# Kernel optimization log

Hardware: AMD Instinct MI355X
Metric: run time of the kernel (lower is better)

Reference implementation:

```python
import jax, jax.numpy as jnp
import numpy as np

L = 8        # num_layers
B = 4        # batch
S = 1024     # seq_len
D = 1024     # hidden_size
H = 16       # num_heads
FC = 4096    # fc_size
NEG = -1e9   # additive causal-mask value (matches torch code's -1000000000.0)


def setup_inputs() -> dict:
    key = jax.random.key(0)
    ks = jax.random.split(key, 12)
    std = 0.02
    inputs = jax.random.normal(ks[0], (B, S, D), jnp.float32)
    # per-layer stacked parameters; torch Linear y = x W^T + b, here stored as [in, out]
    Wq = jax.random.normal(ks[1], (L, D, D), jnp.float32) * std
    Wk = jax.random.normal(ks[2], (L, D, D), jnp.float32) * std
    Wv = jax.random.normal(ks[3], (L, D, D), jnp.float32) * std
    Wo = jax.random.normal(ks[4], (L, D, D), jnp.float32) * std
    W1 = jax.random.normal(ks[5], (L, D, FC), jnp.float32) * std
    W2 = jax.random.normal(ks[6], (L, FC, D), jnp.float32) * std
    bq = jnp.zeros((L, D), jnp.float32)
    bk = jnp.zeros((L, D), jnp.float32)
    bv = jnp.zeros((L, D), jnp.float32)
    bo = jnp.zeros((L, D), jnp.float32)
    b1 = jnp.zeros((L, FC), jnp.float32)
    b2 = jnp.zeros((L, D), jnp.float32)
    ln_g = jnp.ones((D,), jnp.float32)   # single LayerNorm shared across all sites
    ln_b = jnp.zeros((D,), jnp.float32)
    scale = jnp.asarray(0.1, jnp.float32)  # re-zero residual scale (init 0 in torch; 0.1 for non-degenerate test)
    return dict(inputs=inputs, Wq=Wq, bq=bq, Wk=Wk, bk=bk, Wv=Wv, bv=bv,
                Wo=Wo, bo=bo, W1=W1, b1=b1, W2=W2, b2=b2,
                ln_g=ln_g, ln_b=ln_b, scale=scale)


def reference(inputs, Wq, bq, Wk, bk, Wv, bv, Wo, bo, W1, b1, W2, b2, ln_g, ln_b, scale):
    Bz, Sl, Dm = inputs.shape
    nL = Wq.shape[0]
    dh = Dm // H
    inv_sqrt_dh = 1.0 / np.sqrt(dh).astype(np.float32)

    def layer_norm(x):  # shared gamma/beta, eps matches torch default 1e-5
        mu = jnp.mean(x, axis=-1, keepdims=True)
        var = jnp.var(x, axis=-1, keepdims=True)
        return (x - mu) * jax.lax.rsqrt(var + 1e-5) * ln_g + ln_b

    # causal additive bias [S, S], broadcasts over [B, H, S, S]
    bias = jnp.triu(jnp.full((Sl, Sl), NEG, inputs.dtype), k=1)

    x = inputs
    for i in range(nL):
        # --- masked self-attention block ---
        r = layer_norm(x)
        q = (r @ Wq[i] + bq[i]).reshape(Bz, Sl, H, dh)
        k = (r @ Wk[i] + bk[i]).reshape(Bz, Sl, H, dh)
        v = (r @ Wv[i] + bv[i]).reshape(Bz, Sl, H, dh)
        logits = jnp.einsum('bqhd,bkhd->bhqk', q, k) * inv_sqrt_dh + bias
        attn = jax.nn.softmax(logits, axis=-1)
        vals = jnp.einsum('bhqk,bkhd->bqhd', attn, v).reshape(Bz, Sl, Dm)
        r = vals @ Wo[i] + bo[i]
        x = x + scale * r  # re-zero residual (dropout is identity at inference)
        # --- FFN block ---
        r = layer_norm(x)
        r = jax.nn.gelu(r @ W1[i] + b1[i], approximate=False) @ W2[i] + b2[i]
        x = x + scale * r
    return layer_norm(x)
```

## Files before the change

kernel.cpp:

```cpp
#include <hip/hip_runtime.h>


typedef __bf16 bf16x8 __attribute__((ext_vector_type(8)));
typedef float  f32x4  __attribute__((ext_vector_type(4)));
typedef float  f32x16 __attribute__((ext_vector_type(16)));
typedef unsigned int u32x4 __attribute__((ext_vector_type(4)));

#define DEV static __device__ __forceinline__

DEV unsigned short f2bf(float x) {
  unsigned u = __builtin_bit_cast(unsigned int, x);
  u += 0x7fffu + ((u >> 16) & 1u);
  return (unsigned short)(u >> 16);
}

DEV unsigned int pack2bf(float lo, float hi) {
  return (unsigned int)f2bf(lo) | ((unsigned int)f2bf(hi) << 16);
}

DEV f32x4 mfma16(bf16x8 a, bf16x8 b, f32x4 c) {
  return __builtin_amdgcn_mfma_f32_16x16x32_bf16(a, b, c, 0, 0, 0);
}

DEV f32x16 mfma32(bf16x8 a, bf16x8 b, f32x16 c) {
  return __builtin_amdgcn_mfma_f32_32x32x16_bf16(a, b, c, 0, 0, 0);
}

DEV bf16x8 ldb8(const unsigned short* p) {
  return *reinterpret_cast<const bf16x8*>(p);
}

DEV void gload_lds16(const unsigned short* g, unsigned short* l) {
  __builtin_amdgcn_global_load_lds(
      (const __attribute__((address_space(1))) void*)g,
      (__attribute__((address_space(3))) void*)l, 16, 0, 0);
}

__global__ void transpose_cvt(const float* __restrict__ src,
                              unsigned short* __restrict__ dst,
                              int srcStride, int dstStride) {
  __shared__ float tile[32][33];
  const int t  = threadIdx.x;
  const int r  = t >> 3;
  const int c4 = (t & 7) << 2;
  const int k  = blockIdx.x * 32 + r;
  const int n0 = blockIdx.y * 32 + c4;
  const float4 v = *reinterpret_cast<const float4*>(src + (size_t)k * srcStride + n0);
  tile[r][c4] = v.x; tile[r][c4 + 1] = v.y; tile[r][c4 + 2] = v.z; tile[r][c4 + 3] = v.w;
  __syncthreads();
  const int n  = blockIdx.y * 32 + r;
  const int k0 = blockIdx.x * 32 + c4;
  ushort4 o;
  o.x = f2bf(tile[c4][r]);     o.y = f2bf(tile[c4 + 1][r]);
  o.z = f2bf(tile[c4 + 2][r]); o.w = f2bf(tile[c4 + 3][r]);
  *reinterpret_cast<ushort4*>(dst + (size_t)n * dstStride + k0) = o;
}

__global__ void transpose_cvt4(const float* __restrict__ Wq, const float* __restrict__ Wk,
                               const float* __restrict__ Wv, const float* __restrict__ Wo,
                               unsigned short* __restrict__ Wqkv_t,
                               unsigned short* __restrict__ Wo_t) {
  __shared__ float tile[32][33];
  const int z = blockIdx.z;
  const float* src = (z == 0) ? Wq : (z == 1) ? Wk : (z == 2) ? Wv : Wo;
  unsigned short* dst = (z == 3) ? Wo_t : (Wqkv_t + (size_t)z * 1024 * 1024);
  const int t  = threadIdx.x;
  const int r  = t >> 3;
  const int c4 = (t & 7) << 2;
  const int k  = blockIdx.x * 32 + r;
  const int n0 = blockIdx.y * 32 + c4;
  const float4 v = *reinterpret_cast<const float4*>(src + (size_t)k * 1024 + n0);
  tile[r][c4] = v.x; tile[r][c4 + 1] = v.y; tile[r][c4 + 2] = v.z; tile[r][c4 + 3] = v.w;
  __syncthreads();
  const int n  = blockIdx.y * 32 + r;
  const int k0 = blockIdx.x * 32 + c4;
  ushort4 o;
  o.x = f2bf(tile[c4][r]);     o.y = f2bf(tile[c4 + 1][r]);
  o.z = f2bf(tile[c4 + 2][r]); o.w = f2bf(tile[c4 + 3][r]);
  *reinterpret_cast<ushort4*>(dst + (size_t)n * 1024 + k0) = o;
}

__global__ void pack_qkv_bias(const float* __restrict__ bq, const float* __restrict__ bk,
                              const float* __restrict__ bv, float* __restrict__ out) {
  int i = blockIdx.x * 256 + threadIdx.x;
  out[i] = (i < 1024) ? bq[i] : (i < 2048 ? bk[i - 1024] : bv[i - 2048]);
}

template <int OUTF32>
__global__ __launch_bounds__(256) void ln_kernel(
    const float* x, const float* __restrict__ gam,
    const float* __restrict__ bet, void* out) {
  const int t = threadIdx.x, wave = t >> 6, lane = t & 63;
  const int row = blockIdx.x * 4 + wave;
  const float* xr = x + (size_t)row * 1024;
  float4 v[4];
  float s = 0.f, ss = 0.f;
  #pragma unroll
  for (int k = 0; k < 4; ++k) {
    v[k] = *reinterpret_cast<const float4*>(xr + k * 256 + lane * 4);
    s  += v[k].x + v[k].y + v[k].z + v[k].w;
    ss += v[k].x * v[k].x + v[k].y * v[k].y + v[k].z * v[k].z + v[k].w * v[k].w;
  }
  #pragma unroll
  for (int m = 1; m <= 32; m <<= 1) { s += __shfl_xor(s, m); ss += __shfl_xor(ss, m); }
  const float mean = s * (1.0f / 1024.0f);
  const float var  = ss * (1.0f / 1024.0f) - mean * mean;
  const float rstd = rsqrtf(var + 1e-5f);
  #pragma unroll
  for (int k = 0; k < 4; ++k) {
    const float4 g  = *reinterpret_cast<const float4*>(gam + k * 256 + lane * 4);
    const float4 bb = *reinterpret_cast<const float4*>(bet + k * 256 + lane * 4);
    const float y0 = (v[k].x - mean) * rstd * g.x + bb.x;
    const float y1 = (v[k].y - mean) * rstd * g.y + bb.y;
    const float y2 = (v[k].z - mean) * rstd * g.z + bb.z;
    const float y3 = (v[k].w - mean) * rstd * g.w + bb.w;
    if (OUTF32) {
      float4 o; o.x = y0; o.y = y1; o.z = y2; o.w = y3;
      *reinterpret_cast<float4*>((float*)out + (size_t)row * 1024 + k * 256 + lane * 4) = o;
    } else {
      ushort4 o; o.x = f2bf(y0); o.y = f2bf(y1); o.z = f2bf(y2); o.w = f2bf(y3);
      *reinterpret_cast<ushort4*>((unsigned short*)out + (size_t)row * 1024 + k * 256 + lane * 4) = o;
    }
  }
}

template <int MODE>
__global__ __launch_bounds__(512) void gemm8r(
    const unsigned short* __restrict__ A, const unsigned short* __restrict__ Bt,
    const float* __restrict__ bias, unsigned short* __restrict__ outb,
    unsigned short* __restrict__ vT, int N, int K) {
  __shared__ __attribute__((aligned(16))) unsigned short lds[7 * 8192];
  const int t = threadIdx.x, wave = t >> 6, lane = t & 63;
  const int wm = wave >> 2, wn = wave & 3;
  const int rl15 = lane & 15;

  const int nbn = N >> 8;
  const int qq  = gridDim.x >> 3;
  const int swz = (blockIdx.x & 7) * qq + (blockIdx.x >> 3);
  const int m0 = (swz / nbn) << 8, n0 = (swz % nbn) << 8;

  const unsigned short* aG = A  + (size_t)m0 * K;
  const unsigned short* bG = Bt + (size_t)n0 * K;

  const int srow = lane >> 2;
  const int ssl  = (((lane & 3) ^ ((srow >> 1) & 3)) << 3);
  const int swA  = (((lane >> 4) ^ ((lane >> 1) & 3)) << 3);

  auto stageA = [&](int slot, int kt) {
    #pragma unroll
    for (int j = 0; j < 2; ++j) {
      const int c = wave + j * 8;
      gload_lds16(aG + (size_t)(c * 16 + srow) * K + kt * 32 + ssl,
                  &lds[slot * 8192 + c * 512]);
    }
  };
  auto stageB = [&](int slot, int kt) {
    #pragma unroll
    for (int j = 0; j < 2; ++j) {
      const int c = wave + j * 8;
      gload_lds16(bG + (size_t)(c * 16 + srow) * K + kt * 32 + ssl,
                  &lds[slot * 8192 + c * 512]);
    }
  };

  const int nk = K >> 5;
  stageA(0, 0); stageB(1, 0);
  stageA(2, 1); stageB(3, 1);
  asm volatile("s_waitcnt vmcnt(4)" ::: "memory");
  asm volatile("s_barrier" ::: "memory");

  f32x4 acc[8][4] = {};
  int sA = 0, sB = 1, pA = 4, pB = 5;

  for (int kt = 0; kt < nk; ++kt) {
    const bool more = (kt + 2 < nk);
    if (more) { stageA(pA, kt + 2); stageB(pB, kt + 2); }
    const int ab = sA * 8192, bb = sB * 8192;
    bf16x8 af[8], bfr[4];
    #pragma unroll
    for (int mi = 0; mi < 8; ++mi)
      af[mi] = ldb8(&lds[ab + (wm * 128 + mi * 16 + rl15) * 32 + swA]);
    #pragma unroll
    for (int ni = 0; ni < 4; ++ni)
      bfr[ni] = ldb8(&lds[bb + (wn * 64 + ni * 16 + rl15) * 32 + swA]);
    __builtin_amdgcn_s_setprio(1);
    #pragma unroll
    for (int mi = 0; mi < 8; ++mi)
      #pragma unroll
      for (int ni = 0; ni < 4; ++ni)
        acc[mi][ni] = mfma16(af[mi], bfr[ni], acc[mi][ni]);
    __builtin_amdgcn_s_setprio(0);
    if (more) asm volatile("s_waitcnt vmcnt(4)" ::: "memory");
    else      asm volatile("s_waitcnt vmcnt(0)" ::: "memory");
    asm volatile("s_barrier" ::: "memory");
    sA += 2; if (sA >= 7) sA -= 7;
    sB += 2; if (sB >= 7) sB -= 7;
    pA += 2; if (pA >= 7) pA -= 7;
    pB += 2; if (pB >= 7) pB -= 7;
  }

  const int mrow = m0 + wm * 128 + (lane >> 4) * 4;
  const int ncol = n0 + wn * 64 + rl15;
  #pragma unroll
  for (int ni = 0; ni < 4; ++ni) {
    const int n = ncol + ni * 16;
    const float bn = bias[n];
    #pragma unroll
    for (int mi = 0; mi < 8; ++mi) {
      const int row0 = mrow + mi * 16;
      if constexpr (MODE == 3) {
        if (n >= 2048) {
          const int h = (n - 2048) >> 6, d = (n - 2048) & 63;
          const int b = row0 >> 10, s = row0 & 1023;
          ushort4 o;
          o.x = f2bf(acc[mi][ni][0] + bn); o.y = f2bf(acc[mi][ni][1] + bn);
          o.z = f2bf(acc[mi][ni][2] + bn); o.w = f2bf(acc[mi][ni][3] + bn);
          *reinterpret_cast<ushort4*>(vT + ((size_t)(b * 16 + h) * 64 + d) * 1024 + s) = o;
          continue;
        }
      }
      #pragma unroll
      for (int r = 0; r < 4; ++r) {
        const size_t idx = (size_t)(row0 + r) * N + n;
        float v = acc[mi][ni][r] + bn;
        if constexpr (MODE == 1)
          v = 0.5f * v * (1.0f + erff(v * 0.70710678118f));
        outb[idx] = f2bf(v);
      }
    }
  }
}

template <int MODE>
__global__ __launch_bounds__(256) void gemm4k(
    const unsigned short* __restrict__ A, const unsigned short* __restrict__ Bt,
    const float* __restrict__ bias, unsigned short* __restrict__ outb,
    const float* xin, float* xout, const float* __restrict__ scale_p,
    int N, int K) {
  __shared__ __attribute__((aligned(16))) unsigned short lds[36864];
  const int t = threadIdx.x, wave = t >> 6, lane = t & 63;
  const int m0 = blockIdx.x * 128, n0 = blockIdx.y * 64;
  const int wm = wave >> 1, wn = wave & 1;

  int srowA[4], scolA[4];
  #pragma unroll
  for (int j = 0; j < 4; ++j) {
    const int c = j * 256 + wave * 64 + lane;
    const int r = c >> 3;
    srowA[j] = r;
    scolA[j] = ((c & 7) ^ (r & 7)) << 3;
  }
  const unsigned short* aBase = A + (size_t)m0 * K;
  const unsigned short* bBase = Bt + (size_t)n0 * K;

  const int xk0 = (((lane >> 4)    ) ^ (lane & 7)) << 3;
  const int xk1 = (((lane >> 4) | 4) ^ (lane & 7)) << 3;
  const int arow = (wm * 64 + (lane & 15)) * 64;
  const int brow = (wn * 32 + (lane & 15)) * 64;

  auto stage = [&](int slot, int kt) {
    unsigned short* lA = &lds[slot * 8192];
    unsigned short* lB = &lds[24576 + slot * 4096];
    const int ko = kt * 64;
    #pragma unroll
    for (int j = 0; j < 4; ++j)
      gload_lds16(aBase + (size_t)srowA[j] * K + ko + scolA[j],
                  lA + j * 2048 + wave * 512);
    #pragma unroll
    for (int j = 0; j < 2; ++j)
      gload_lds16(bBase + (size_t)srowA[j] * K + ko + scolA[j],
                  lB + j * 2048 + wave * 512);
  };

  f32x4 acc[4][2] = {};
  const int nk = K >> 6;

  stage(0, 0); stage(1, 1);
  asm volatile("s_waitcnt vmcnt(6)" ::: "memory");
  asm volatile("s_barrier" ::: "memory");

  int cs = 0;
  for (int kt = 0; kt < nk; ++kt) {
    const bool more = (kt + 2 < nk);
    if (more) { int ps = cs + 2; if (ps >= 3) ps -= 3; stage(ps, kt + 2); }
    const unsigned short* lA = &lds[cs * 8192];
    const unsigned short* lB = &lds[24576 + cs * 4096];
    #pragma unroll
    for (int kc = 0; kc < 2; ++kc) {
      const int xk = kc ? xk1 : xk0;
      bf16x8 a[4], b[2];
      #pragma unroll
      for (int mi = 0; mi < 4; ++mi) a[mi] = ldb8(&lA[arow + mi * 1024 + xk]);
      #pragma unroll
      for (int ni = 0; ni < 2; ++ni) b[ni] = ldb8(&lB[brow + ni * 1024 + xk]);
      __builtin_amdgcn_s_setprio(1);
      #pragma unroll
      for (int mi = 0; mi < 4; ++mi)
        #pragma unroll
        for (int ni = 0; ni < 2; ++ni)
          acc[mi][ni] = mfma16(a[mi], b[ni], acc[mi][ni]);
      __builtin_amdgcn_s_setprio(0);
    }
    if (more) asm volatile("s_waitcnt vmcnt(6)" ::: "memory");
    else      asm volatile("s_waitcnt vmcnt(0)" ::: "memory");
    asm volatile("s_barrier" ::: "memory");
    ++cs; if (cs == 3) cs = 0;
  }

  const int mrow = m0 + wm * 64 + (lane >> 4) * 4;
  const int ncol = n0 + wn * 32 + (lane & 15);
  float scl = 0.f;
  if constexpr (MODE == 2) scl = scale_p[0];
  #pragma unroll
  for (int ni = 0; ni < 2; ++ni) {
    const int n = ncol + ni * 16;
    const float bn = bias[n];
    #pragma unroll
    for (int mi = 0; mi < 4; ++mi) {
      #pragma unroll
      for (int r = 0; r < 4; ++r) {
        const size_t idx = (size_t)(mrow + mi * 16 + r) * N + n;
        float v = acc[mi][ni][r] + bn;
        if constexpr (MODE == 2) {
          xout[idx] = xin[idx] + scl * v;
        } else {
          outb[idx] = f2bf(v);
        }
      }
    }
  }
}

__global__ __launch_bounds__(256) void attn_kernel(
    const unsigned short* __restrict__ qkv, const unsigned short* __restrict__ vT,
    unsigned short* __restrict__ vals) {
  const int bh = blockIdx.x & 63;
  const int qb = 7 - (blockIdx.x >> 6);
  const int b = bh >> 4, h = bh & 15;
  const int t = threadIdx.x, wave = t >> 6, lane = t & 63;
  const int l31 = lane & 31, hi = lane >> 5;
  const int q0w = qb * 128 + wave * 32;
  const int diag = q0w >> 6;
  const int nkt = qb * 2 + 2;

  __shared__ __attribute__((aligned(16))) unsigned short ldsK[2][4096];
  __shared__ __attribute__((aligned(16))) unsigned short ldsV[2][4096];

  const unsigned short* qkvB  = qkv + (size_t)b * 1024 * 3072;
  const unsigned short* vHead = vT + (size_t)bh * 64 * 1024;

  const int c0row = t >> 3, c0ch = t & 7;
  const int c1row = (t + 256) >> 3, c1ch = t & 7;
  const int s0col = ((c0ch ^ (c0row & 7)) << 3);
  const int s1col = ((c1ch ^ (c1row & 7)) << 3);
  const int wbase = (t >> 6) * 512;

  auto stageKV = [&](int buf, int kt) {
    const int kv0 = kt * 64;
    gload_lds16(qkvB + (size_t)(kv0 + c0row) * 3072 + 1024 + h * 64 + s0col,
                &ldsK[buf][wbase]);
    gload_lds16(qkvB + (size_t)(kv0 + c1row) * 3072 + 1024 + h * 64 + s1col,
                &ldsK[buf][2048 + wbase]);
    gload_lds16(vHead + (size_t)c0row * 1024 + kv0 + s0col, &ldsV[buf][wbase]);
    gload_lds16(vHead + (size_t)c1row * 1024 + kv0 + s1col, &ldsV[buf][2048 + wbase]);
  };

  const unsigned short* qrow = qkvB + (size_t)(q0w + l31) * 3072 + h * 64 + hi * 8;
  bf16x8 qf[4];
  #pragma unroll
  for (int s = 0; s < 4; ++s) qf[s] = ldb8(qrow + 16 * s);

  f32x16 oacc[2] = {};
  float mrun = -1e30f, lrun = 0.f;

  stageKV(0, 0);
  __syncthreads();

  for (int kt = 0; kt < nkt; ++kt) {
    const int cur = kt & 1;
    if (kt + 1 < nkt) stageKV(cur ^ 1, kt + 1);
    if (kt <= diag) {
      const unsigned short* K = ldsK[cur];
      const unsigned short* V = ldsV[cur];
      #pragma unroll
      for (int sub = 0; sub < 2; ++sub) {
        const int krow = sub * 32 + l31;
        f32x16 sacc = {};
        #pragma unroll
        for (int s = 0; s < 4; ++s) {
          const bf16x8 kf = ldb8(&K[krow * 64 + (((2 * s + hi) ^ (krow & 7)) << 3)]);
          sacc = mfma32(kf, qf[s], sacc);
        }
        float p[16];
        #pragma unroll
        for (int r = 0; r < 16; ++r) p[r] = sacc[r] * 0.125f;
        if (kt == diag) {
          const int qg = q0w + l31;
          #pragma unroll
          for (int r = 0; r < 16; ++r) {
            const int kv = kt * 64 + sub * 32 + (r & 3) + 8 * (r >> 2) + 4 * hi;
            if (kv > qg) p[r] = -1e30f;
          }
        }
        float mloc = p[0];
        #pragma unroll
        for (int r = 1; r < 16; ++r) mloc = fmaxf(mloc, p[r]);
        mloc = fmaxf(mloc, __shfl_xor(mloc, 32));
        const float mnew = fmaxf(mrun, mloc);
        const float facq = __expf(mrun - mnew);
        mrun = mnew;
        float sloc = 0.f;
        #pragma unroll
        for (int r = 0; r < 16; ++r) {
          const float e = __expf(p[r] - mnew);
          p[r] = e;
          sloc += e;
        }
        sloc += __shfl_xor(sloc, 32);
        lrun = lrun * facq + sloc;
        #pragma unroll
        for (int db = 0; db < 2; ++db)
          #pragma unroll
          for (int r = 0; r < 16; ++r) oacc[db][r] *= facq;
        unsigned int w[8], x[8];
        #pragma unroll
        for (int i = 0; i < 8; ++i) w[i] = pack2bf(p[2 * i], p[2 * i + 1]);
        #pragma unroll
        for (int i = 0; i < 8; ++i) x[i] = (unsigned)__shfl_xor((int)w[i], 32);
        #pragma unroll
        for (int ks = 0; ks < 2; ++ks) {
          const int qi = 2 * ks + hi;
          u32x4 fu;
          if (hi) { fu = u32x4{x[2 * qi], x[2 * qi + 1], w[2 * qi], w[2 * qi + 1]}; }
          else    { fu = u32x4{w[2 * qi], w[2 * qi + 1], x[2 * qi], x[2 * qi + 1]}; }
          const bf16x8 pf = __builtin_bit_cast(bf16x8, fu);
          #pragma unroll
          for (int db = 0; db < 2; ++db) {
            const int vrow = db * 32 + l31;
            const int vch  = sub * 4 + ks * 2 + hi;
            const bf16x8 vf = ldb8(&V[vrow * 64 + ((vch ^ (vrow & 7)) << 3)]);
            oacc[db] = mfma32(vf, pf, oacc[db]);
          }
        }
      }
    }
    __syncthreads();
  }

  const float rl = 1.0f / lrun;
  const size_t qrowOut = (size_t)(b * 1024 + q0w + l31) * 1024 + h * 64;
  #pragma unroll
  for (int db = 0; db < 2; ++db)
    #pragma unroll
    for (int rq = 0; rq < 4; ++rq) {
      const int d0 = db * 32 + 8 * rq + 4 * hi;
      ushort4 o;
      o.x = f2bf(oacc[db][rq * 4 + 0] * rl);
      o.y = f2bf(oacc[db][rq * 4 + 1] * rl);
      o.z = f2bf(oacc[db][rq * 4 + 2] * rl);
      o.w = f2bf(oacc[db][rq * 4 + 3] * rl);
      *reinterpret_cast<ushort4*>(vals + qrowOut + d0) = o;
    }
}

extern "C" void kernel_launch(void* const* d_in, const int* in_sizes, int n_in,
                              void* d_out, int out_size, void* d_ws, size_t ws_size,
                              hipStream_t stream) {
  (void)in_sizes; (void)n_in; (void)out_size; (void)ws_size;
  const float* inputs = (const float*)d_in[0];
  const float* Wq = (const float*)d_in[1];  const float* bq = (const float*)d_in[2];
  const float* Wk = (const float*)d_in[3];  const float* bk = (const float*)d_in[4];
  const float* Wv = (const float*)d_in[5];  const float* bv = (const float*)d_in[6];
  const float* Wo = (const float*)d_in[7];  const float* bo = (const float*)d_in[8];
  const float* W1 = (const float*)d_in[9];  const float* b1 = (const float*)d_in[10];
  const float* W2 = (const float*)d_in[11]; const float* b2 = (const float*)d_in[12];
  const float* ln_g = (const float*)d_in[13];
  const float* ln_b = (const float*)d_in[14];
  const float* scale_p = (const float*)d_in[15];
  float* xbuf = (float*)d_out;

  char* w = (char*)d_ws;
  size_t off = 0;
  auto take = [&](size_t bytes) {
    void* p = w + off;
    off = (off + bytes + 255) & ~(size_t)255;
    return p;
  };
  unsigned short* Wqkv_t = (unsigned short*)take((size_t)3072 * 1024 * 2);
  unsigned short* Wo_t   = (unsigned short*)take((size_t)1024 * 1024 * 2);
  unsigned short* W1_t   = (unsigned short*)take((size_t)4096 * 1024 * 2);
  unsigned short* W2_t   = (unsigned short*)take((size_t)1024 * 4096 * 2);
  float*          bqkv   = (float*)take(3072 * 4);
  unsigned short* rbuf   = (unsigned short*)take((size_t)4096 * 1024 * 2);
  unsigned short* qkvb   = (unsigned short*)take((size_t)4096 * 3072 * 2);
  unsigned short* vTb    = (unsigned short*)take((size_t)64 * 64 * 1024 * 2);
  unsigned short* valsb  = (unsigned short*)take((size_t)4096 * 1024 * 2);
  unsigned short* hbuf   = (unsigned short*)take((size_t)4096 * 4096 * 2);

  for (int i = 0; i < 8; ++i) {
    const float* xin = (i == 0) ? inputs : xbuf;
    transpose_cvt4<<<dim3(32, 32, 4), 256, 0, stream>>>(
        Wq + (size_t)i * 1024 * 1024, Wk + (size_t)i * 1024 * 1024,
        Wv + (size_t)i * 1024 * 1024, Wo + (size_t)i * 1024 * 1024, Wqkv_t, Wo_t);
    transpose_cvt<<<dim3(32, 128), 256, 0, stream>>>(W1 + (size_t)i * 1024 * 4096, W1_t, 4096, 1024);
    transpose_cvt<<<dim3(128, 32), 256, 0, stream>>>(W2 + (size_t)i * 4096 * 1024, W2_t, 1024, 4096);
    pack_qkv_bias<<<12, 256, 0, stream>>>(bq + i * 1024, bk + i * 1024, bv + i * 1024, bqkv);
    ln_kernel<0><<<1024, 256, 0, stream>>>(xin, ln_g, ln_b, rbuf);
    gemm8r<3><<<192, 512, 0, stream>>>(rbuf, Wqkv_t, bqkv, qkvb, vTb, 3072, 1024);
    attn_kernel<<<512, 256, 0, stream>>>(qkvb, vTb, valsb);
    gemm4k<2><<<dim3(32, 16), 256, 0, stream>>>(valsb, Wo_t, bo + i * 1024, nullptr,
                                                xin, xbuf, scale_p, 1024, 1024);
    ln_kernel<0><<<1024, 256, 0, stream>>>(xbuf, ln_g, ln_b, rbuf);
    gemm8r<1><<<256, 512, 0, stream>>>(rbuf, W1_t, b1 + i * 4096, hbuf, nullptr, 4096, 1024);
    gemm4k<2><<<dim3(32, 16), 256, 0, stream>>>(hbuf, W2_t, b2 + i * 1024, nullptr,
                                                xbuf, xbuf, scale_p, 1024, 4096);
  }
  ln_kernel<1><<<1024, 256, 0, stream>>>(xbuf, ln_g, ln_b, xbuf);
}
```

Measured before the change: 1.808 ms.

## Merge per-layer weight prep kernels and deepen gemm8r prefetch to three stages

Four per-layer prep launches (QKV/O transpose, W1 transpose, W2 transpose, bias pack) become one prep_layer kernel that dispatches on block index, cutting launch count and tail gaps. The gemm8r LDS ring goes from 7 to 8 slots so three k-tiles are prefetched instead of two. Slot indices now come from a power-of-two mask, and the vmcnt waits are adjusted for the deeper pipeline. The larger LDS footprint (128KB) may limit occupancy, and the wait counts must match the number of outstanding loads exactly.

```diff
diff --git a/kernel.cpp b/kernel.cpp
--- a/kernel.cpp
+++ b/kernel.cpp
@@ -36,54 +36,50 @@
       (__attribute__((address_space(3))) void*)l, 16, 0, 0);
 }
 
-__global__ void transpose_cvt(const float* __restrict__ src,
-                              unsigned short* __restrict__ dst,
-                              int srcStride, int dstStride) {
-  __shared__ float tile[32][33];
-  const int t  = threadIdx.x;
-  const int r  = t >> 3;
-  const int c4 = (t & 7) << 2;
-  const int k  = blockIdx.x * 32 + r;
-  const int n0 = blockIdx.y * 32 + c4;
+__global__ __launch_bounds__(256) void prep_layer(
+    const float* __restrict__ Wq, const float* __restrict__ Wk,
+    const float* __restrict__ Wv, const float* __restrict__ Wo,
+    const float* __restrict__ W1, const float* __restrict__ W2,
+    const float* __restrict__ bq, const float* __restrict__ bk,
+    const float* __restrict__ bv,
+    unsigned short* __restrict__ Wqkv_t, unsigned short* __restrict__ Wo_t,
+    unsigned short* __restrict__ W1_t, unsigned short* __restrict__ W2_t,
+    float* __restrict__ bqkv) {
+  const int bid = blockIdx.x;
+  const int t = threadIdx.x;
+  if (bid >= 12288) {
+    const int i = (bid - 12288) * 256 + t;
+    bqkv[i] = (i < 1024) ? bq[i] : (i < 2048 ? bk[i - 1024] : bv[i - 2048]);
+    return;
+  }
+  const float* src;
+  unsigned short* dst;
+  int kt, nt, srcStride, dstStride;
+  if (bid < 4096) {
+    const int z = bid >> 10, tile = bid & 1023;
+    src = (z == 0) ? Wq : (z == 1) ? Wk : (z == 2) ? Wv : Wo;
+    dst = (z == 3) ? Wo_t : (Wqkv_t + (size_t)z * 1024 * 1024);
+    kt = tile >> 5; nt = tile & 31; srcStride = 1024; dstStride = 1024;
+  } else if (bid < 8192) {
+    const int tile = bid - 4096;
+    src = W1; dst = W1_t;
+    kt = tile >> 7; nt = tile & 127; srcStride = 4096; dstStride = 1024;
+  } else {
+    const int tile = bid - 8192;
+    src = W2; dst = W2_t;
+    kt = tile >> 5; nt = tile & 31; srcStride = 1024; dstStride = 4096;
+  }
+  __shared__ float ts[32][33];
+  const int r = t >> 3, c4 = (t & 7) << 2;
+  const int k = kt * 32 + r, n0 = nt * 32 + c4;
   const float4 v = *reinterpret_cast<const float4*>(src + (size_t)k * srcStride + n0);
-  tile[r][c4] = v.x; tile[r][c4 + 1] = v.y; tile[r][c4 + 2] = v.z; tile[r][c4 + 3] = v.w;
+  ts[r][c4] = v.x; ts[r][c4 + 1] = v.y; ts[r][c4 + 2] = v.z; ts[r][c4 + 3] = v.w;
   __syncthreads();
-  const int n  = blockIdx.y * 32 + r;
-  const int k0 = blockIdx.x * 32 + c4;
+  const int n = nt * 32 + r, k0 = kt * 32 + c4;
   ushort4 o;
-  o.x = f2bf(tile[c4][r]);     o.y = f2bf(tile[c4 + 1][r]);
-  o.z = f2bf(tile[c4 + 2][r]); o.w = f2bf(tile[c4 + 3][r]);
+  o.x = f2bf(ts[c4][r]);     o.y = f2bf(ts[c4 + 1][r]);
+  o.z = f2bf(ts[c4 + 2][r]); o.w = f2bf(ts[c4 + 3][r]);
   *reinterpret_cast<ushort4*>(dst + (size_t)n * dstStride + k0) = o;
-}
-
-__global__ void transpose_cvt4(const float* __restrict__ Wq, const float* __restrict__ Wk,
-                               const float* __restrict__ Wv, const float* __restrict__ Wo,
-                               unsigned short* __restrict__ Wqkv_t,
-                               unsigned short* __restrict__ Wo_t) {
-  __shared__ float tile[32][33];
-  const int z = blockIdx.z;
-  const float* src = (z == 0) ? Wq : (z == 1) ? Wk : (z == 2) ? Wv : Wo;
-  unsigned short* dst = (z == 3) ? Wo_t : (Wqkv_t + (size_t)z * 1024 * 1024);
-  const int t  = threadIdx.x;
-  const int r  = t >> 3;
-  const int c4 = (t & 7) << 2;
-  const int k  = blockIdx.x * 32 + r;
-  const int n0 = blockIdx.y * 32 + c4;
-  const float4 v = *reinterpret_cast<const float4*>(src + (size_t)k * 1024 + n0);
-  tile[r][c4] = v.x; tile[r][c4 + 1] = v.y; tile[r][c4 + 2] = v.z; tile[r][c4 + 3] = v.w;
-  __syncthreads();
-  const int n  = blockIdx.y * 32 + r;
-  const int k0 = blockIdx.x * 32 + c4;
-  ushort4 o;
-  o.x = f2bf(tile[c4][r]);     o.y = f2bf(tile[c4 + 1][r]);
-  o.z = f2bf(tile[c4 + 2][r]); o.w = f2bf(tile[c4 + 3][r]);
-  *reinterpret_cast<ushort4*>(dst + (size_t)n * 1024 + k0) = o;
-}
-
-__global__ void pack_qkv_bias(const float* __restrict__ bq, const float* __restrict__ bk,
-                              const float* __restrict__ bv, float* __restrict__ out) {
-  int i = blockIdx.x * 256 + threadIdx.x;
-  out[i] = (i < 1024) ? bq[i] : (i < 2048 ? bk[i - 1024] : bv[i - 2048]);
 }
 
 template <int OUTF32>
@@ -129,7 +125,7 @@
     const unsigned short* __restrict__ A, const unsigned short* __restrict__ Bt,
     const float* __restrict__ bias, unsigned short* __restrict__ outb,
     unsigned short* __restrict__ vT, int N, int K) {
-  __shared__ __attribute__((aligned(16))) unsigned short lds[7 * 8192];
+  __shared__ __attribute__((aligned(16))) unsigned short lds[8 * 8192];
   const int t = threadIdx.x, wave = t >> 6, lane = t & 63;
   const int wm = wave >> 2, wn = wave & 3;
   const int rl15 = lane & 15;
@@ -166,16 +162,18 @@
   const int nk = K >> 5;
   stageA(0, 0); stageB(1, 0);
   stageA(2, 1); stageB(3, 1);
-  asm volatile("s_waitcnt vmcnt(4)" ::: "memory");
+  stageA(4, 2); stageB(5, 2);
+  asm volatile("s_waitcnt vmcnt(8)" ::: "memory");
   asm volatile("s_barrier" ::: "memory");
 
   f32x4 acc[8][4] = {};
-  int sA = 0, sB = 1, pA = 4, pB = 5;
 
   for (int kt = 0; kt < nk; ++kt) {
-    const bool more = (kt + 2 < nk);
-    if (more) { stageA(pA, kt + 2); stageB(pB, kt + 2); }
-    const int ab = sA * 8192, bb = sB * 8192;
+    if (kt + 3 < nk) {
+      const int p = (2 * (kt + 3)) & 7;
+      stageA(p, kt + 3); stageB(p + 1, kt + 3);
+    }
+    const int ab = ((2 * kt) & 7) * 8192, bb = ab + 8192;
     bf16x8 af[8], bfr[4];
     #pragma unroll
     for (int mi = 0; mi < 8; ++mi)
@@ -190,13 +188,10 @@
       for (int ni = 0; ni < 4; ++ni)
         acc[mi][ni] = mfma16(af[mi], bfr[ni], acc[mi][ni]);
     __builtin_amdgcn_s_setprio(0);
-    if (more) asm volatile("s_waitcnt vmcnt(4)" ::: "memory");
-    else      asm volatile("s_waitcnt vmcnt(0)" ::: "memory");
+    if (kt + 3 < nk)      asm volatile("s_waitcnt vmcnt(8)" ::: "memory");
+    else if (kt + 2 < nk) asm volatile("s_waitcnt vmcnt(4)" ::: "memory");
+    else                  asm volatile("s_waitcnt vmcnt(0)" ::: "memory");
     asm volatile("s_barrier" ::: "memory");
-    sA += 2; if (sA >= 7) sA -= 7;
-    sB += 2; if (sB >= 7) sB -= 7;
-    pA += 2; if (pA >= 7) pA -= 7;
-    pB += 2; if (pB >= 7) pB -= 7;
   }
 
   const int mrow = m0 + wm * 128 + (lane >> 4) * 4;
@@ -499,12 +494,12 @@
 
   for (int i = 0; i < 8; ++i) {
     const float* xin = (i == 0) ? inputs : xbuf;
-    transpose_cvt4<<<dim3(32, 32, 4), 256, 0, stream>>>(
+    prep_layer<<<12300, 256, 0, stream>>>(
         Wq + (size_t)i * 1024 * 1024, Wk + (size_t)i * 1024 * 1024,
-        Wv + (size_t)i * 1024 * 1024, Wo + (size_t)i * 1024 * 1024, Wqkv_t, Wo_t);
-    transpose_cvt<<<dim3(32, 128), 256, 0, stream>>>(W1 + (size_t)i * 1024 * 4096, W1_t, 4096, 1024);
-    transpose_cvt<<<dim3(128, 32), 256, 0, stream>>>(W2 + (size_t)i * 4096 * 1024, W2_t, 1024, 4096);
-    pack_qkv_bias<<<12, 256, 0, stream>>>(bq + i * 1024, bk + i * 1024, bv + i * 1024, bqkv);
+        Wv + (size_t)i * 1024 * 1024, Wo + (size_t)i * 1024 * 1024,
+        W1 + (size_t)i * 1024 * 4096, W2 + (size_t)i * 4096 * 1024,
+        bq + i * 1024, bk + i * 1024, bv + i * 1024,
+        Wqkv_t, Wo_t, W1_t, W2_t, bqkv);
     ln_kernel<0><<<1024, 256, 0, stream>>>(xin, ln_g, ln_b, rbuf);
     gemm8r<3><<<192, 512, 0, stream>>>(rbuf, Wqkv_t, bqkv, qkvb, vTb, 3072, 1024);
     attn_kernel<<<512, 256, 0, stream>>>(qkvb, vTb, valsb);
```

Result: faster. 1.755 ms, median of 3 (-2.9%).
